# Kernel optimization log

Hardware: AMD Instinct MI355X
Metric: run time of the kernel (lower is better)

The kernel has to match this reference:

```python
import jax, jax.numpy as jnp
import numpy as np
from jax.scipy.special import logsumexp

REG = 0.1
ITERS = 10
TEMP = 0.1
W = 0.5            # cross_domain_weight
NEG = -1000000.0   # mask fill value used by the torch module
EPS = 1e-12        # F.normalize eps


def setup_inputs() -> dict:
    key = jax.random.key(0)
    k1, k2, k3, k4, k5 = jax.random.split(key, 5)
    n, n_ex, m, L, h = 64, 4, 49, 32, 512
    x = jax.random.normal(k1, (n * n_ex, m, h), jnp.float32)
    y = jax.random.normal(k2, (n, L, h), jnp.float32)
    lengths = jax.random.randint(k3, (n,), 8, L + 1)
    y_mask = jnp.arange(L)[None, :] >= lengths[:, None]  # True = padded token
    dustbin_im = 0.1 * jax.random.normal(k4, (1, 1, 1), jnp.float32)
    dustbin_lang = 0.1 * jax.random.normal(k5, (1, 1, 1), jnp.float32)
    return {"x": x, "y": y, "dustbin_im": dustbin_im,
            "dustbin_lang": dustbin_lang, "y_mask": y_mask}


def _l2norm(t):
    return t / jnp.maximum(jnp.linalg.norm(t, axis=-1, keepdims=True), EPS)


def _log_sinkhorn(Z, log_mu, log_nu, mask_cols, iters, reg):
    # Z: (b, m+1, n+1); mask_cols: (b, n+1) bool, True = invalid column
    u = jnp.zeros_like(log_mu)
    v = jnp.where(mask_cols, NEG, jnp.zeros_like(log_nu))
    pen = mask_cols[:, None, :].astype(Z.dtype) * 1e6

    def body(carry, _):
        u, v = carry
        M = (Z + u[:, :, None] + v[:, None, :]) / reg
        u = u + reg * (log_mu - logsumexp(M, axis=2))
        M = (Z + u[:, :, None] + v[:, None, :]) / reg
        v_new = v + reg * (log_nu - logsumexp(M + pen, axis=1))
        v = jnp.where(mask_cols, NEG, v_new)
        return (u, v), None

    (u, v), _ = jax.lax.scan(body, (u, v), None, length=iters)
    return (Z + u[:, :, None] + v[:, None, :]) / reg


def reference(x, y, dustbin_im, dustbin_lang, y_mask):
    n, L, h = y.shape
    n_ex = x.shape[0] // n
    m = x.shape[1]
    b = n * n * n_ex

    xn = _l2norm(x)   # (n*n_ex, m, h)
    yn = _l2norm(y)   # (n, L, h)
    # equivalent to repeat_interleave(x, n) vs repeat(y, n*n_ex): index i*n + j
    scores = jnp.einsum('imh,jlh->ijml', xn, yn).reshape(b, m, L)

    mask_cols = jnp.tile(y_mask, (n * n_ex, 1))                       # (b, L)
    mask_cols = jnp.concatenate([mask_cols, jnp.zeros((b, 1), bool)], axis=1)  # (b, L+1)
    scores_mask = jnp.broadcast_to(mask_cols[:, None, :], (b, m + 1, L + 1))

    a_im = jnp.clip(dustbin_im, -1.0, 1.0)
    a_lang = jnp.clip(dustbin_lang, -1.0, 1.0)
    bins0 = jnp.broadcast_to(a_im, (b, m, 1))
    bins1 = jnp.broadcast_to(a_lang, (b, 1, L))
    alpha = jnp.broadcast_to(a_im, (b, 1, 1))
    couplings = jnp.concatenate(
        [jnp.concatenate([scores, bins0], axis=2),
         jnp.concatenate([bins1, alpha], axis=2)], axis=1)            # (b, m+1, L+1)
    couplings = jnp.where(scores_mask, NEG, couplings)

    ms = jnp.asarray(m, scores.dtype)
    ns = (~scores_mask).sum(axis=(1, 2)).astype(scores.dtype) / (m + 1) - 1  # valid tokens per row
    norm = -jnp.log(ms + ns)                                          # (b,)
    log_mu = jnp.concatenate(
        [jnp.broadcast_to(norm[:, None], (b, m)), (jnp.log(ns) + norm)[:, None]], axis=1)
    log_nu = jnp.concatenate(
        [jnp.broadcast_to(norm[:, None], (b, L)), (jnp.log(ms) + norm)[:, None]], axis=1)
    log_nu = jnp.where(mask_cols, NEG, log_nu)

    Zlog = _log_sinkhorn(couplings, log_mu, log_nu, mask_cols, ITERS, REG)
    Zm = jnp.exp(Zlog - norm[:, None, None])                          # transport plan
    ot_scores = (scores * Zm[:, :-1, :-1]).sum(axis=(1, 2)) / TEMP    # (b,)

    scores2 = ot_scores.reshape(n * n_ex, n)
    matching = Zm.reshape(n * n_ex, n, m + 1, L + 1)

    idx = jnp.arange(n * n_ex)
    grp = idx // n_ex                                                 # lang index of image i
    pos = scores2[idx, grp]                                           # (n*n_ex,)
    # InfoNCE by language: pos vs all other langs for each image (full row)
    loss_lang = -(pos - logsumexp(scores2, axis=1)).mean()
    # InfoNCE by image: pos vs out-of-group images for the same lang
    cols = scores2.T[grp]                                             # (n*n_ex, n*n_ex), row i = scores2[:, grp[i]]
    allowed = (idx[None, :] // n_ex != grp[:, None]) | (idx[None, :] == idx[:, None])
    lse_im = logsumexp(jnp.where(allowed, cols, -jnp.inf), axis=1)
    loss_im = -(pos - lse_im).mean()
    loss = W * loss_lang + (1.0 - W) * loss_im
    return matching, loss
```

## Files before the change

kernel.cpp:

```cpp
#include <hip/hip_runtime.h>
#include <math.h>

#define XROWS 12544
#define YROWS 2048
#define HD 512
#define NM 49
#define NL 32
#define MP1 50
#define LP1 33
#define BSTRIDE 1650
#define INVREG 10.0f
#define ZSTR 1652

typedef __attribute__((ext_vector_type(8))) short short8;
typedef __attribute__((ext_vector_type(4))) float floatx4;
typedef _Float16 half2_t __attribute__((ext_vector_type(2)));

__device__ __forceinline__ unsigned short f2bf(float f) {
    unsigned int u = __builtin_bit_cast(unsigned int, f);
    u = (u + 0x7FFFu + ((u >> 16) & 1u)) >> 16;
    return (unsigned short)u;
}

__device__ __forceinline__ void gload_lds16(const void* g, void* l) {
    typedef const __attribute__((address_space(1))) unsigned int* gp_t;
    typedef __attribute__((address_space(3))) unsigned int* lp_t;
    __builtin_amdgcn_global_load_lds((gp_t)g, (lp_t)l, 16, 0, 0);
}

__device__ __forceinline__ float rl(float v, int l) {
    return __builtin_bit_cast(float, __builtin_amdgcn_readlane(__builtin_bit_cast(int, v), l));
}
__device__ __forceinline__ half2_t rlh2(unsigned v, int l) {
    return __builtin_bit_cast(half2_t, (unsigned)__builtin_amdgcn_readlane((int)v, l));
}
__device__ __forceinline__ float fdot2(half2_t a, half2_t b, float c) {
    return __builtin_amdgcn_fdot2(a, b, c, false);
}

__global__ __launch_bounds__(256) void normcvt_kernel(
    const float* __restrict__ x, const float* __restrict__ y,
    unsigned short* __restrict__ xb, unsigned short* __restrict__ yb)
{
    const int wid = blockIdx.x * 4 + (threadIdx.x >> 6);
    const int lane = threadIdx.x & 63;
    if (wid >= XROWS + YROWS) return;
    const float* src;
    unsigned short* dst;
    if (wid < XROWS) { src = x + (size_t)wid * HD;           dst = xb + (size_t)wid * HD; }
    else             { src = y + (size_t)(wid - XROWS) * HD; dst = yb + (size_t)(wid - XROWS) * HD; }
    const float4 v0 = *(const float4*)(src + lane * 8);
    const float4 v1 = *(const float4*)(src + lane * 8 + 4);
    float s = v0.x*v0.x + v0.y*v0.y + v0.z*v0.z + v0.w*v0.w
            + v1.x*v1.x + v1.y*v1.y + v1.z*v1.z + v1.w*v1.w;
    #pragma unroll
    for (int o = 32; o > 0; o >>= 1) s += __shfl_xor(s, o, 64);
    const float inv = 1.0f / fmaxf(sqrtf(s), 1e-12f);
    short8 ov;
    ov[0] = (short)f2bf(v0.x * inv); ov[1] = (short)f2bf(v0.y * inv);
    ov[2] = (short)f2bf(v0.z * inv); ov[3] = (short)f2bf(v0.w * inv);
    ov[4] = (short)f2bf(v1.x * inv); ov[5] = (short)f2bf(v1.y * inv);
    ov[6] = (short)f2bf(v1.z * inv); ov[7] = (short)f2bf(v1.w * inv);
    *(short8*)(dst + lane * 8) = ov;
}

__global__ __launch_bounds__(512) void fused_kernel(
    const unsigned short* __restrict__ xb, const unsigned short* __restrict__ yb,
    const int* __restrict__ ymask,
    const float* __restrict__ d_im, const float* __restrict__ d_lang,
    float* __restrict__ outZ, float* __restrict__ scores2)
{
    const int wv   = threadIdx.x >> 6;
    const int lane = threadIdx.x & 63;
    const int i  = blockIdx.x & 255;
    const int jg = blockIdx.x >> 8;
    const int j  = jg * 8 + wv;
    const int pair = i * 64 + j;
    __shared__ alignas(16) float LDSU[8 * ZSTR];
    char* XSB = (char*)LDSU;
    float* zs = LDSU + wv * ZSTR;
    float* base = outZ + (size_t)pair * BSTRIDE;

    #pragma unroll
    for (int pass = 0; pass < 7; ++pass) {
        const int row = pass * 8 + wv;
        if (row < NM)
            gload_lds16(xb + ((size_t)i * NM + row) * HD + lane * 8, XSB + row * 1040);
    }
    __syncthreads();

    const int mval = (lane < NL) ? (ymask[j * NL + lane] != 0) : 1;
    const unsigned long long vbm = __ballot(lane < NL && !mval);
    const float ns = (float)__popcll(vbm);
    const float kim   = __expf(fminf(fmaxf(d_im[0],   -1.f), 1.f) * INVREG);
    const float klang = __expf(fminf(fmaxf(d_lang[0], -1.f), 1.f) * INVREG);

    const int la = lane & 15;
    const int koff = (lane >> 4) * 8;
    const unsigned short* yr0 = yb + ((size_t)j * NL + la) * HD + koff;
    const unsigned short* yr1 = yr0 + 16 * HD;

    floatx4 acc[4][2] = {};
    #pragma unroll
    for (int kt = 0; kt < 16; ++kt) {
        const int kb = (kt * 32 + koff) * 2;
        const short8 a0 = *(const short8*)(XSB + (0  + la) * 1040 + kb);
        const short8 a1 = *(const short8*)(XSB + (16 + la) * 1040 + kb);
        const short8 a2 = *(const short8*)(XSB + (32 + la) * 1040 + kb);
        const short8 a3 = *(const short8*)(XSB + 48 * 1040 + kb);
        const short8 b0 = *(const short8*)(yr0 + kt * 32);
        const short8 b1 = *(const short8*)(yr1 + kt * 32);
        acc[0][0] = __builtin_amdgcn_mfma_f32_16x16x32_bf16(a0, b0, acc[0][0], 0, 0, 0);
        acc[0][1] = __builtin_amdgcn_mfma_f32_16x16x32_bf16(a0, b1, acc[0][1], 0, 0, 0);
        acc[1][0] = __builtin_amdgcn_mfma_f32_16x16x32_bf16(a1, b0, acc[1][0], 0, 0, 0);
        acc[1][1] = __builtin_amdgcn_mfma_f32_16x16x32_bf16(a1, b1, acc[1][1], 0, 0, 0);
        acc[2][0] = __builtin_amdgcn_mfma_f32_16x16x32_bf16(a2, b0, acc[2][0], 0, 0, 0);
        acc[2][1] = __builtin_amdgcn_mfma_f32_16x16x32_bf16(a2, b1, acc[2][1], 0, 0, 0);
        acc[3][0] = __builtin_amdgcn_mfma_f32_16x16x32_bf16(a3, b0, acc[3][0], 0, 0, 0);
        acc[3][1] = __builtin_amdgcn_mfma_f32_16x16x32_bf16(a3, b1, acc[3][1], 0, 0, 0);
    }
    __syncthreads();

    #pragma unroll
    for (int mi = 0; mi < 4; ++mi) {
        #pragma unroll
        for (int q = 0; q < 4; ++q) {
            const int row = mi * 16 + (lane >> 4) * 4 + q;
            if (row < MP1) {
                zs[row * 33 + la]      = acc[mi][0][q];
                zs[row * 33 + 16 + la] = acc[mi][1][q];
            }
        }
    }
    asm volatile("s_waitcnt lgkmcnt(0)" ::: "memory");
    __builtin_amdgcn_sched_barrier(0);

    float krf[33];
    #pragma unroll
    for (int c = 0; c < 33; ++c) krf[c] = 0.f;
    if (lane < NM) {
        #pragma unroll
        for (int c = 0; c < NL; ++c) {
            const float sc = zs[lane * 33 + c];
            krf[c] = ((vbm >> c) & 1ull) ? __expf(sc * INVREG) : 0.f;
        }
    } else if (lane == NM) {
        #pragma unroll
        for (int c = 0; c < NL; ++c) krf[c] = ((vbm >> c) & 1ull) ? klang : 0.f;
    }
    krf[32] = kim;
    asm volatile("s_waitcnt lgkmcnt(0)" ::: "memory");
    __builtin_amdgcn_sched_barrier(0);

    half2_t kr2[17];
    #pragma unroll
    for (int q = 0; q < 16; ++q) {
        half2_t h; h[0] = (_Float16)krf[2*q]; h[1] = (_Float16)krf[2*q+1];
        kr2[q] = h;
    }
    { half2_t h; h[0] = (_Float16)krf[32]; h[1] = (_Float16)0.f; kr2[16] = h; }

    unsigned short* T = (unsigned short*)zs;
    if (lane < MP1) {
        #pragma unroll
        for (int c = 0; c < 33; ++c)
            T[c * 52 + lane] = __builtin_bit_cast(unsigned short, (_Float16)krf[c]);
    }
    asm volatile("s_waitcnt lgkmcnt(0)" ::: "memory");
    __builtin_amdgcn_sched_barrier(0);
    half2_t kc2[25];
    {
        const int tb = ((lane < LP1) ? lane : 0) * 52;
        #pragma unroll
        for (int q = 0; q < 25; ++q)
            kc2[q] = __builtin_bit_cast(half2_t, *(const unsigned*)(T + tb + 2*q));
    }

    const float mup = (lane < NM) ? 1.f : ns;
    const float nup = (lane < NL) ? 1.f : 49.f;
    const bool colA = (lane < NL) ? (((vbm >> lane) & 1ull) != 0ull) : (lane == NL);
    float eu = 0.f;
    float ev = colA ? 1.f : 0.f;

    for (int it = 0; it < 10; ++it) {
        const float evn = __shfl_xor(ev, 1, 64);
        half2_t evp; evp[0] = (_Float16)ev; evp[1] = (_Float16)evn;
        const unsigned evpu = __builtin_bit_cast(unsigned, evp);
        float a0 = 0.f, a1 = 0.f;
        #pragma unroll
        for (int q = 0; q < 17; q += 2) {
            a0 = fdot2(kr2[q], rlh2(evpu, 2*q), a0);
            if (q + 1 < 17) a1 = fdot2(kr2[q+1], rlh2(evpu, 2*q+2), a1);
        }
        eu = __fdividef(mup, a0 + a1);

        const float eun = __shfl_xor(eu, 1, 64);
        half2_t eup; eup[0] = (_Float16)eu; eup[1] = (_Float16)eun;
        const unsigned eupu = __builtin_bit_cast(unsigned, eup);
        float b0 = 0.f, b1 = 0.f;
        #pragma unroll
        for (int q = 0; q < 25; q += 2) {
            b0 = fdot2(kc2[q], rlh2(eupu, 2*q), b0);
            if (q + 1 < 25) b1 = fdot2(kc2[q+1], rlh2(eupu, 2*q+2), b1);
        }
        const float Sv = b0 + b1;
        ev = colA ? __fdividef(nup, Sv) : 0.f;
    }

    const float ev32 = rl(ev, 32);
    const float eu49 = rl(eu, 49);
    const float evA  = __shfl(ev, la, 64);
    const float evB  = __shfl(ev, 16 + la, 64);
    float ot = 0.f;
    #pragma unroll
    for (int mi = 0; mi < 4; ++mi) {
        #pragma unroll
        for (int q = 0; q < 4; ++q) {
            const int row = mi * 16 + ((lane >> 4) << 2) + q;
            const float eur = __shfl(eu, row, 64);
            if (row < NM) {
                const float s0 = acc[mi][0][q];
                const float s1 = acc[mi][1][q];
                const float zm0 = __expf(s0 * INVREG) * eur * evA;
                const float zm1 = __expf(s1 * INVREG) * eur * evB;
                zs[row * 33 + la]      = zm0;
                zs[row * 33 + 16 + la] = zm1;
                ot = fmaf(s0 * INVREG, zm0, fmaf(s1 * INVREG, zm1, ot));
            }
        }
    }
    if (lane < MP1) zs[lane * 33 + 32] = kim * eu * ev32;
    if (lane < LP1) {
        const float kd = (lane < NL) ? (((vbm >> lane) & 1ull) ? klang : 0.f) : kim;
        zs[NM * 33 + lane] = kd * eu49 * ev;
    }
    #pragma unroll
    for (int o = 32; o > 0; o >>= 1) ot += __shfl_xor(ot, o, 64);
    if (lane == 0) scores2[pair] = ot;
    asm volatile("s_waitcnt lgkmcnt(0)" ::: "memory");
    __builtin_amdgcn_sched_barrier(0);
    #pragma unroll
    for (int t = 0; t < 13; ++t) {
        const int idx = t * 64 + lane;
        if (idx < 825) *(float2*)(base + idx * 2) = *(const float2*)&zs[idx * 2];
    }
}

__global__ __launch_bounds__(256) void loss_kernel(
    const float* __restrict__ s2, float* __restrict__ out)
{
    __shared__ float S2[16384];
    const int tid = threadIdx.x;
    for (int t = tid; t < 4096; t += 256)
        ((float4*)S2)[t] = ((const float4*)s2)[t];
    __syncthreads();

    const int i = tid;
    const int g = i >> 2;
    const float pos = S2[i * 64 + g];
    float mx = -3.0e38f;
    for (int jj = 0; jj < 64; ++jj) {
        const int c = (jj + i) & 63;
        mx = fmaxf(mx, S2[i * 64 + c]);
    }
    float sm = 0.f;
    for (int jj = 0; jj < 64; ++jj) {
        const int c = (jj + i) & 63;
        sm += __expf(S2[i * 64 + c] - mx);
    }
    const float lse1 = __logf(sm) + mx;

    float mx2 = -3.0e38f;
    for (int k = 0; k < 256; ++k) {
        const bool allowed = ((k >> 2) != g) || (k == i);
        if (allowed) mx2 = fmaxf(mx2, S2[k * 64 + g]);
    }
    float sm2 = 0.f;
    for (int k = 0; k < 256; ++k) {
        const bool allowed = ((k >> 2) != g) || (k == i);
        if (allowed) sm2 += __expf(S2[k * 64 + g] - mx2);
    }
    const float lse2 = __logf(sm2) + mx2;

    float li = 0.5f * (lse1 - pos) + 0.5f * (lse2 - pos);
    #pragma unroll
    for (int o = 32; o > 0; o >>= 1) li += __shfl_xor(li, o, 64);
    __shared__ float wred[4];
    if ((i & 63) == 0) wred[i >> 6] = li;
    __syncthreads();
    if (i == 0) out[0] = (wred[0] + wred[1] + wred[2] + wred[3]) * (1.0f / 256.0f);
}

extern "C" void kernel_launch(void* const* d_in, const int* in_sizes, int n_in,
                              void* d_out, int out_size, void* d_ws, size_t ws_size,
                              hipStream_t stream)
{
    const float* x      = (const float*)d_in[0];
    const float* y      = (const float*)d_in[1];
    const float* d_im   = (const float*)d_in[2];
    const float* d_lang = (const float*)d_in[3];
    const int* ymask    = (const int*)d_in[4];
    float* out = (float*)d_out;
    float* ws  = (float*)d_ws;

    float* s2          = ws;
    unsigned short* xb = (unsigned short*)(ws + 16384);
    unsigned short* yb = xb + (size_t)XROWS * HD;

    normcvt_kernel<<<(XROWS + YROWS + 3) / 4, 256, 0, stream>>>(x, y, xb, yb);
    fused_kernel<<<2048, 512, 0, stream>>>(xb, yb, ymask, d_im, d_lang, out, s2);
    loss_kernel<<<1, 256, 0, stream>>>(s2, out + (size_t)16384 * BSTRIDE);
}
```

Measured before the change: 140.9 us.

## Compute kernel exps from MFMA registers and share column LSE in loss kernel

The main kernel now computes exp(score/reg) straight from the MFMA accumulators into registers and writes the fp16 transposed kernel matrix directly to shared memory. This drops the fp32 score staging round-trip and one barrier stage, and the register copies are reused in the final transport-plan step instead of recomputing exp. Half conversions in the Sinkhorn loop use the packed cvt_pkrtz intrinsic, which rounds toward zero rather than to nearest. The loss kernel precomputes a per-column max and out-of-group sum once, so each row adds only its positive term instead of scanning 256 entries twice. The extra register arrays raise register pressure.

```diff
diff --git a/kernel.cpp b/kernel.cpp
--- a/kernel.cpp
+++ b/kernel.cpp
@@ -20,6 +20,9 @@
     unsigned int u = __builtin_bit_cast(unsigned int, f);
     u = (u + 0x7FFFu + ((u >> 16) & 1u)) >> 16;
     return (unsigned short)u;
+}
+__device__ __forceinline__ unsigned short f16b(float v) {
+    return __builtin_bit_cast(unsigned short, (_Float16)v);
 }
 
 __device__ __forceinline__ void gload_lds16(const void* g, void* l) {
@@ -121,53 +124,55 @@
     }
     __syncthreads();
 
-    #pragma unroll
-    for (int mi = 0; mi < 4; ++mi) {
+    unsigned short* T = (unsigned short*)zs;
+    const bool mA = (vbm >> la) & 1ull;
+    const bool mB = (vbm >> (16 + la)) & 1ull;
+    float kA[16], kB[16];
+    #pragma unroll
+    for (int mi = 0; mi < 3; ++mi)
         #pragma unroll
         for (int q = 0; q < 4; ++q) {
-            const int row = mi * 16 + (lane >> 4) * 4 + q;
-            if (row < MP1) {
-                zs[row * 33 + la]      = acc[mi][0][q];
-                zs[row * 33 + 16 + la] = acc[mi][1][q];
-            }
-        }
-    }
+            kA[mi*4+q] = mA ? __expf(acc[mi][0][q] * INVREG) : 0.f;
+            kB[mi*4+q] = mB ? __expf(acc[mi][1][q] * INVREG) : 0.f;
+        }
+    kA[12] = mA ? __expf(acc[3][0][0] * INVREG) : 0.f;
+    kB[12] = mB ? __expf(acc[3][1][0] * INVREG) : 0.f;
+    kA[13] = kA[14] = kA[15] = 0.f;
+    kB[13] = kB[14] = kB[15] = 0.f;
+
+    #pragma unroll
+    for (int mi = 0; mi < 3; ++mi) {
+        const int r0 = mi * 16 + ((lane >> 4) << 2);
+        ushort4 wa, wb;
+        wa.x = f16b(kA[mi*4+0]); wa.y = f16b(kA[mi*4+1]);
+        wa.z = f16b(kA[mi*4+2]); wa.w = f16b(kA[mi*4+3]);
+        wb.x = f16b(kB[mi*4+0]); wb.y = f16b(kB[mi*4+1]);
+        wb.z = f16b(kB[mi*4+2]); wb.w = f16b(kB[mi*4+3]);
+        *(ushort4*)(T + la * 52 + r0)        = wa;
+        *(ushort4*)(T + (16 + la) * 52 + r0) = wb;
+    }
+    if ((lane >> 4) == 0) {
+        T[la * 52 + 48]        = f16b(kA[12]);
+        T[(16 + la) * 52 + 48] = f16b(kB[12]);
+    }
+    if (lane < NL)       T[lane * 52 + 49] = f16b(((vbm >> lane) & 1ull) ? klang : 0.f);
+    else if (lane == NL) T[32 * 52 + 49]   = f16b(kim);
+    if (lane < NM)       T[32 * 52 + lane] = f16b(kim);
     asm volatile("s_waitcnt lgkmcnt(0)" ::: "memory");
     __builtin_amdgcn_sched_barrier(0);
 
-    float krf[33];
-    #pragma unroll
-    for (int c = 0; c < 33; ++c) krf[c] = 0.f;
-    if (lane < NM) {
-        #pragma unroll
-        for (int c = 0; c < NL; ++c) {
-            const float sc = zs[lane * 33 + c];
-            krf[c] = ((vbm >> c) & 1ull) ? __expf(sc * INVREG) : 0.f;
-        }
-    } else if (lane == NM) {
-        #pragma unroll
-        for (int c = 0; c < NL; ++c) krf[c] = ((vbm >> c) & 1ull) ? klang : 0.f;
-    }
-    krf[32] = kim;
-    asm volatile("s_waitcnt lgkmcnt(0)" ::: "memory");
-    __builtin_amdgcn_sched_barrier(0);
-
     half2_t kr2[17];
-    #pragma unroll
-    for (int q = 0; q < 16; ++q) {
-        half2_t h; h[0] = (_Float16)krf[2*q]; h[1] = (_Float16)krf[2*q+1];
-        kr2[q] = h;
-    }
-    { half2_t h; h[0] = (_Float16)krf[32]; h[1] = (_Float16)0.f; kr2[16] = h; }
-
-    unsigned short* T = (unsigned short*)zs;
-    if (lane < MP1) {
-        #pragma unroll
-        for (int c = 0; c < 33; ++c)
-            T[c * 52 + lane] = __builtin_bit_cast(unsigned short, (_Float16)krf[c]);
-    }
-    asm volatile("s_waitcnt lgkmcnt(0)" ::: "memory");
-    __builtin_amdgcn_sched_barrier(0);
+    {
+        const int p = (lane < MP1) ? lane : 0;
+        #pragma unroll
+        for (int q = 0; q < 16; ++q) {
+            const unsigned lo = T[(2*q)   * 52 + p];
+            const unsigned hi = T[(2*q+1) * 52 + p];
+            kr2[q] = __builtin_bit_cast(half2_t, lo | (hi << 16));
+        }
+        half2_t h; h[0] = (_Float16)kim; h[1] = (_Float16)0.f;
+        kr2[16] = h;
+    }
     half2_t kc2[25];
     {
         const int tb = ((lane < LP1) ? lane : 0) * 52;
@@ -184,8 +189,8 @@
 
     for (int it = 0; it < 10; ++it) {
         const float evn = __shfl_xor(ev, 1, 64);
-        half2_t evp; evp[0] = (_Float16)ev; evp[1] = (_Float16)evn;
-        const unsigned evpu = __builtin_bit_cast(unsigned, evp);
+        const auto evp_ = __builtin_amdgcn_cvt_pkrtz(ev, evn);
+        const unsigned evpu = __builtin_bit_cast(unsigned, evp_);
         float a0 = 0.f, a1 = 0.f;
         #pragma unroll
         for (int q = 0; q < 17; q += 2) {
@@ -195,8 +200,8 @@
         eu = __fdividef(mup, a0 + a1);
 
         const float eun = __shfl_xor(eu, 1, 64);
-        half2_t eup; eup[0] = (_Float16)eu; eup[1] = (_Float16)eun;
-        const unsigned eupu = __builtin_bit_cast(unsigned, eup);
+        const auto eup_ = __builtin_amdgcn_cvt_pkrtz(eu, eun);
+        const unsigned eupu = __builtin_bit_cast(unsigned, eup_);
         float b0 = 0.f, b1 = 0.f;
         #pragma unroll
         for (int q = 0; q < 25; q += 2) {
@@ -221,8 +226,8 @@
             if (row < NM) {
                 const float s0 = acc[mi][0][q];
                 const float s1 = acc[mi][1][q];
-                const float zm0 = __expf(s0 * INVREG) * eur * evA;
-                const float zm1 = __expf(s1 * INVREG) * eur * evB;
+                const float zm0 = kA[mi*4+q] * eur * evA;
+                const float zm1 = kB[mi*4+q] * eur * evB;
                 zs[row * 33 + la]      = zm0;
                 zs[row * 33 + 16 + la] = zm1;
                 ot = fmaf(s0 * INVREG, zm0, fmaf(s1 * INVREG, zm1, ot));
@@ -250,9 +255,24 @@
     const float* __restrict__ s2, float* __restrict__ out)
 {
     __shared__ float S2[16384];
+    __shared__ float colmax[64], colsum[64];
+    __shared__ float wred[4];
     const int tid = threadIdx.x;
     for (int t = tid; t < 4096; t += 256)
         ((float4*)S2)[t] = ((const float4*)s2)[t];
+    __syncthreads();
+
+    const int gc = tid >> 2, sc = tid & 3;
+    float cm = -3.0e38f;
+    for (int k = sc * 64; k < sc * 64 + 64; ++k) cm = fmaxf(cm, S2[k * 64 + gc]);
+    cm = fmaxf(cm, __shfl_xor(cm, 1, 64));
+    cm = fmaxf(cm, __shfl_xor(cm, 2, 64));
+    float cs = 0.f;
+    for (int k = sc * 64; k < sc * 64 + 64; ++k)
+        if ((k >> 2) != gc) cs += __expf(S2[k * 64 + gc] - cm);
+    cs += __shfl_xor(cs, 1, 64);
+    cs += __shfl_xor(cs, 2, 64);
+    if (sc == 0) { colmax[gc] = cm; colsum[gc] = cs; }
     __syncthreads();
 
     const int i = tid;
@@ -270,22 +290,12 @@
     }
     const float lse1 = __logf(sm) + mx;
 
-    float mx2 = -3.0e38f;
-    for (int k = 0; k < 256; ++k) {
-        const bool allowed = ((k >> 2) != g) || (k == i);
-        if (allowed) mx2 = fmaxf(mx2, S2[k * 64 + g]);
-    }
-    float sm2 = 0.f;
-    for (int k = 0; k < 256; ++k) {
-        const bool allowed = ((k >> 2) != g) || (k == i);
-        if (allowed) sm2 += __expf(S2[k * 64 + g] - mx2);
-    }
-    const float lse2 = __logf(sm2) + mx2;
+    const float cmg = colmax[g], csg = colsum[g];
+    const float lse2 = __logf(csg + __expf(pos - cmg)) + cmg;
 
     float li = 0.5f * (lse1 - pos) + 0.5f * (lse2 - pos);
     #pragma unroll
     for (int o = 32; o > 0; o >>= 1) li += __shfl_xor(li, o, 64);
-    __shared__ float wred[4];
     if ((i & 63) == 0) wred[i >> 6] = li;
     __syncthreads();
     if (i == 0) out[0] = (wred[0] + wred[1] + wred[2] + wred[3]) * (1.0f / 256.0f);
```

New measurement: 145.5 us. 3.2% more time.
